# Kernel optimization log

Hardware: AMD Instinct MI355X
Metric: run time of the kernel (lower is better)

The kernel has to match this reference:

```python
import jax, jax.numpy as jnp
import numpy as np

B, T, C, H = 2, 2048, 1024, 16
D = C // H  # head_dim = 64

def setup_inputs() -> dict:
    key = jax.random.key(0)
    k1, k2, k3 = jax.random.split(key, 3)
    x = jax.random.normal(k1, (B, T, C), dtype=jnp.float32)
    W_attn = jax.random.normal(k2, (C, 3 * C), dtype=jnp.float32) * (1.0 / np.sqrt(C))
    W_proj = jax.random.normal(k3, (C, C), dtype=jnp.float32) * (1.0 / np.sqrt(C))
    return {"x": x, "W_attn": W_attn, "W_proj": W_proj}

def reference(x, W_attn, W_proj):
    b, t, c = x.shape
    qkv = x @ W_attn                       # [B,T,3C]
    q, k, v = jnp.split(qkv, 3, axis=-1)
    # [B,T,C] -> [B,H,T,D]
    q = q.reshape(b, t, H, D).transpose(0, 2, 1, 3)
    k = k.reshape(b, t, H, D).transpose(0, 2, 1, 3)
    v = v.reshape(b, t, H, D).transpose(0, 2, 1, 3)
    scale = 1.0 / np.sqrt(D).astype(np.float32)
    att = jnp.einsum('bhqd,bhkd->bhqk', q, k) * scale   # [B,H,T,T]
    causal = jnp.tril(jnp.ones((t, t), dtype=bool))
    att = jnp.where(causal[None, None], att, -jnp.inf)
    att = jax.nn.softmax(att, axis=-1)
    y = jnp.einsum('bhqk,bhkd->bhqd', att, v)           # [B,H,T,D]
    y = y.transpose(0, 2, 1, 3).reshape(b, t, c)        # [B,T,C]
    return y @ W_proj
```

## Files before the change

### kernel.cpp

```cpp
#include <hip/hip_runtime.h>
#include <hip/hip_bf16.h>
#include <cstdint>
#include <cstddef>
#include <cmath>

typedef __attribute__((ext_vector_type(8))) short short8v;
typedef __attribute__((ext_vector_type(4))) float f32x4;
typedef __attribute__((ext_vector_type(4))) unsigned short ushort4v;

__device__ __forceinline__ unsigned short f2bf(float f) {
  union { float f; uint32_t u; } v; v.f = f;
  uint32_t u = v.u;
  return (unsigned short)((u + 0x7fffu + ((u >> 16) & 1u)) >> 16);
}

__device__ __forceinline__ float bf2f(unsigned short u) {
  union { uint32_t u; float f; } v; v.u = ((uint32_t)u) << 16; return v.f;
}

__device__ __forceinline__ uint32_t pack2bf(float a, float b) {
  __hip_bfloat162 h = __float22bfloat162_rn(make_float2(a, b));
  union { __hip_bfloat162 h; uint32_t u; } c; c.h = h; return c.u;
}

__device__ __forceinline__ void load_lds_16B(const void* g, void* l) {
  __builtin_amdgcn_global_load_lds((const __attribute__((address_space(1))) void*)g,
                                   (__attribute__((address_space(3))) void*)l, 16, 0, 0);
}

__global__ __launch_bounds__(256) void cvt_bf16_kernel(const float* __restrict__ src,
                                                       unsigned short* __restrict__ dst,
                                                       int n8) {
  int i = blockIdx.x * 256 + threadIdx.x;
  if (i >= n8) return;
  const float4* s4 = (const float4*)src + (size_t)i * 2;
  float4 f0 = s4[0], f1 = s4[1];
  short8v o;
  o[0] = (short)f2bf(f0.x); o[1] = (short)f2bf(f0.y);
  o[2] = (short)f2bf(f0.z); o[3] = (short)f2bf(f0.w);
  o[4] = (short)f2bf(f1.x); o[5] = (short)f2bf(f1.y);
  o[6] = (short)f2bf(f1.z); o[7] = (short)f2bf(f1.w);
  *(short8v*)(dst + (size_t)i * 8) = o;
}

__global__ __launch_bounds__(256) void transpose_bf16_kernel(const float* __restrict__ W,
                                                             unsigned short* __restrict__ WT,
                                                             int K, int N) {
  __shared__ float tile[64][65];
  int n0 = blockIdx.x * 64, k0 = blockIdx.y * 64;
  int tid = threadIdx.x;
#pragma unroll
  for (int i = 0; i < 4; ++i) {
    int idx = i * 256 + tid;
    int r = idx >> 4, c4 = (idx & 15) * 4;
    float4 v = *(const float4*)(W + (size_t)(k0 + r) * N + n0 + c4);
    tile[r][c4] = v.x; tile[r][c4 + 1] = v.y; tile[r][c4 + 2] = v.z; tile[r][c4 + 3] = v.w;
  }
  __syncthreads();
#pragma unroll
  for (int i = 0; i < 4; ++i) {
    int idx = i * 256 + tid;
    int nr = idx >> 4, k4 = (idx & 15) * 4;
    ushort4 o;
    o.x = f2bf(tile[k4 + 0][nr]);
    o.y = f2bf(tile[k4 + 1][nr]);
    o.z = f2bf(tile[k4 + 2][nr]);
    o.w = f2bf(tile[k4 + 3][nr]);
    *(ushort4*)(WT + (size_t)(n0 + nr) * K + k0 + k4) = o;
  }
}

__global__ __launch_bounds__(256) void transpose_v_kernel(const unsigned short* __restrict__ qkv,
                                                          unsigned short* __restrict__ VT) {
  int bid = blockIdx.x;
  int b = bid >> 9, h = (bid >> 5) & 15, tc = bid & 31;
  __shared__ unsigned short tile[64][68];
  int tid = threadIdx.x;
  const unsigned short* src = qkv + (size_t)(b * 2048 + tc * 64) * 3072 + 2048 + h * 64;
#pragma unroll
  for (int p = 0; p < 4; ++p) {
    int idx = p * 256 + tid;
    int r = idx >> 4, c4 = (idx & 15) * 4;
    *(ushort4*)&tile[r][c4] = *(const ushort4*)(src + (size_t)r * 3072 + c4);
  }
  __syncthreads();
  unsigned short* dst = VT + (size_t)(b * 16 + h) * 64 * 2048 + tc * 64;
#pragma unroll
  for (int p = 0; p < 4; ++p) {
    int idx = p * 256 + tid;
    int d = idx >> 4, k = idx & 15;
    int t4 = k * 4;
    int c4 = ((k >> 3) << 5) | ((k & 3) << 3) | (k & 4);
    ushort4 o;
    o.x = tile[t4][d]; o.y = tile[t4 + 1][d]; o.z = tile[t4 + 2][d]; o.w = tile[t4 + 3][d];
    *(ushort4*)(dst + (size_t)d * 2048 + c4) = o;
  }
}

template <int BF16OUT>
__global__ __launch_bounds__(256) void gemm_bt_kernel(const unsigned short* __restrict__ A,
                                                      const unsigned short* __restrict__ BT,
                                                      void* __restrict__ Cout,
                                                      int M, int N, int K) {
  __shared__ __align__(16) char lds[32768];
  char* As = lds;
  char* Bs = lds + 16384;

  int nbn = N >> 7;
  int nwg = gridDim.x;
  int wg = blockIdx.x;
  int per = nwg >> 3;
  int swz = (wg & 7) * per + (wg >> 3);
  int tm = swz / nbn, tn = swz % nbn;

  int tid = threadIdx.x;
  int wid = tid >> 6, lane = tid & 63;
  int l15 = lane & 15, lhi = lane >> 4;
  int wm = wid >> 1, wn = wid & 1;

  const unsigned short* Abase = A + (size_t)(tm * 128) * K;
  const unsigned short* Bbase = BT + (size_t)(tn * 128) * K;

  size_t ofs[4];
#pragma unroll
  for (int i = 0; i < 4; ++i) {
    int row = i * 32 + (tid >> 3);
    int ss = (tid & 7) ^ (row & 7);
    ofs[i] = (size_t)row * K + ss * 8;
  }

  f32x4 acc[4][4] = {};

  for (int kt = 0; kt < K; kt += 64) {
    __syncthreads();
#pragma unroll
    for (int i = 0; i < 4; ++i)
      load_lds_16B(Abase + ofs[i] + kt, As + i * 4096 + tid * 16);
#pragma unroll
    for (int i = 0; i < 4; ++i)
      load_lds_16B(Bbase + ofs[i] + kt, Bs + i * 4096 + tid * 16);
    __syncthreads();

#pragma unroll
    for (int ks = 0; ks < 2; ++ks) {
      short8v af[4], bfr[4];
#pragma unroll
      for (int mi = 0; mi < 4; ++mi) {
        int row = wm * 64 + mi * 16 + l15;
        int ss = (ks * 4 + lhi) ^ (row & 7);
        af[mi] = *(const short8v*)(As + row * 128 + ss * 16);
      }
#pragma unroll
      for (int ni = 0; ni < 4; ++ni) {
        int row = wn * 64 + ni * 16 + l15;
        int ss = (ks * 4 + lhi) ^ (row & 7);
        bfr[ni] = *(const short8v*)(Bs + row * 128 + ss * 16);
      }
#pragma unroll
      for (int mi = 0; mi < 4; ++mi)
#pragma unroll
        for (int ni = 0; ni < 4; ++ni)
          acc[mi][ni] = __builtin_amdgcn_mfma_f32_16x16x32_bf16(af[mi], bfr[ni], acc[mi][ni], 0, 0, 0);
    }
  }

#pragma unroll
  for (int mi = 0; mi < 4; ++mi)
#pragma unroll
    for (int ni = 0; ni < 4; ++ni)
#pragma unroll
      for (int r = 0; r < 4; ++r) {
        int row = tm * 128 + wm * 64 + mi * 16 + lhi * 4 + r;
        int col = tn * 128 + wn * 64 + ni * 16 + l15;
        float v = acc[mi][ni][r];
        if (BF16OUT)
          ((unsigned short*)Cout)[(size_t)row * N + col] = f2bf(v);
        else
          ((float*)Cout)[(size_t)row * N + col] = v;
      }
}

__global__ __launch_bounds__(256) void gemm_bt64_kernel(const unsigned short* __restrict__ A,
                                                        const unsigned short* __restrict__ BT,
                                                        float* __restrict__ Cout,
                                                        int M, int N, int K) {
  __shared__ __align__(16) char lds[24576];
  char* As = lds;
  char* Bs = lds + 8192;

  int nbn = N >> 7;
  int nwg = gridDim.x;
  int wg = blockIdx.x;
  int per = nwg >> 3;
  int swz = (wg & 7) * per + (wg >> 3);
  int tm = swz / nbn, tn = swz % nbn;

  int tid = threadIdx.x;
  int wid = tid >> 6, lane = tid & 63;
  int l15 = lane & 15, lhi = lane >> 4;

  const unsigned short* Abase = A + (size_t)(tm * 64) * K;
  const unsigned short* Bbase = BT + (size_t)(tn * 128) * K;

  size_t ofsA[2], ofsB[4];
#pragma unroll
  for (int i = 0; i < 2; ++i) {
    int row = i * 32 + (tid >> 3);
    int ss = (tid & 7) ^ (row & 7);
    ofsA[i] = (size_t)row * K + ss * 8;
  }
#pragma unroll
  for (int i = 0; i < 4; ++i) {
    int row = i * 32 + (tid >> 3);
    int ss = (tid & 7) ^ (row & 7);
    ofsB[i] = (size_t)row * K + ss * 8;
  }

  f32x4 acc[4][2] = {};

  for (int kt = 0; kt < K; kt += 64) {
    __syncthreads();
#pragma unroll
    for (int i = 0; i < 2; ++i)
      load_lds_16B(Abase + ofsA[i] + kt, As + i * 4096 + tid * 16);
#pragma unroll
    for (int i = 0; i < 4; ++i)
      load_lds_16B(Bbase + ofsB[i] + kt, Bs + i * 4096 + tid * 16);
    __syncthreads();

#pragma unroll
    for (int ks = 0; ks < 2; ++ks) {
      short8v af[4], bfr[2];
#pragma unroll
      for (int mi = 0; mi < 4; ++mi) {
        int row = mi * 16 + l15;
        int ss = (ks * 4 + lhi) ^ (row & 7);
        af[mi] = *(const short8v*)(As + row * 128 + ss * 16);
      }
#pragma unroll
      for (int ni = 0; ni < 2; ++ni) {
        int row = wid * 32 + ni * 16 + l15;
        int ss = (ks * 4 + lhi) ^ (row & 7);
        bfr[ni] = *(const short8v*)(Bs + row * 128 + ss * 16);
      }
#pragma unroll
      for (int mi = 0; mi < 4; ++mi)
#pragma unroll
        for (int ni = 0; ni < 2; ++ni)
          acc[mi][ni] = __builtin_amdgcn_mfma_f32_16x16x32_bf16(af[mi], bfr[ni], acc[mi][ni], 0, 0, 0);
    }
  }

#pragma unroll
  for (int mi = 0; mi < 4; ++mi)
#pragma unroll
    for (int ni = 0; ni < 2; ++ni)
#pragma unroll
      for (int r = 0; r < 4; ++r) {
        int row = tm * 64 + mi * 16 + lhi * 4 + r;
        int col = tn * 128 + wid * 32 + ni * 16 + l15;
        Cout[(size_t)row * N + col] = acc[mi][ni][r];
      }
}


__device__ __forceinline__ short8v scale_q(short8v q) {
  short8v r;
#pragma unroll
  for (int j = 0; j < 8; ++j)
    r[j] = (short)f2bf(bf2f((unsigned short)q[j]) * 0.18033688f);
  return r;
}

__device__ __forceinline__ void mask_diag(f32x4 s[4], int q_abs, int k0, int lhi) {
#pragma unroll
  for (int ni = 0; ni < 4; ++ni)
#pragma unroll
    for (int r = 0; r < 4; ++r) {
      int kv = k0 + ni * 16 + lhi * 4 + r;
      if (kv > q_abs) s[ni][r] = -1e30f;
    }
}

__device__ __forceinline__ void exp_p(f32x4 s[4]) {
#pragma unroll
  for (int ni = 0; ni < 4; ++ni)
#pragma unroll
    for (int r = 0; r < 4; ++r)
      s[ni][r] = exp2f(s[ni][r]);
}

__device__ __forceinline__ void repack_pa(const f32x4 s[4], short8v pa[2]) {
#pragma unroll
  for (int ks = 0; ks < 2; ++ks) {
    union { uint32_t u[4]; short8v v; } pk;
    pk.u[0] = pack2bf(s[2 * ks][0], s[2 * ks][1]);
    pk.u[1] = pack2bf(s[2 * ks][2], s[2 * ks][3]);
    pk.u[2] = pack2bf(s[2 * ks + 1][0], s[2 * ks + 1][1]);
    pk.u[3] = pack2bf(s[2 * ks + 1][2], s[2 * ks + 1][3]);
    pa[ks] = pk.v;
  }
}

__global__ __launch_bounds__(256, 2) void attn_kernel(const unsigned short* __restrict__ qkv,
                                                      const unsigned short* __restrict__ VT,
                                                      unsigned short* __restrict__ yb) {
  const int T = 2048, LD = 3072;
  int bid = blockIdx.x;
  int xcd = bid & 7, ii = bid >> 3;
  int bh = xcd * 4 + (ii & 3);
  int j = ii >> 2;
  int b = bh >> 4, h = bh & 15;
  int qtA = j, qtB = 31 - j;

  int tid = threadIdx.x;
  int wid = tid >> 6, lane = tid & 63;
  int l15 = lane & 15, lhi = lane >> 4;

  __shared__ __align__(16) char Ks[4][8192];
  __shared__ __align__(16) char Vt[4][8192];

  union { uint32_t u[4]; short8v v; } ob;
  ob.u[0] = ob.u[1] = ob.u[2] = ob.u[3] = 0x3F803F80u;
  const short8v onesv = ob.v;

  int qrowA = qtA * 64 + wid * 16 + l15;
  int qrowB = qtB * 64 + wid * 16 + l15;
  const unsigned short* qpA = qkv + (size_t)(b * T + qrowA) * LD + h * 64;
  const unsigned short* qpB = qkv + (size_t)(b * T + qrowB) * LD + h * 64;
  short8v qfA[2], qfB[2];
  qfA[0] = scale_q(*(const short8v*)(qpA + lhi * 8));
  qfA[1] = scale_q(*(const short8v*)(qpA + 32 + lhi * 8));
  qfB[0] = scale_q(*(const short8v*)(qpB + lhi * 8));
  qfB[1] = scale_q(*(const short8v*)(qpB + 32 + lhi * 8));

  const unsigned short* kbase = qkv + (size_t)b * T * LD + 1024 + h * 64;
  const unsigned short* vtbase = VT + (size_t)(b * 16 + h) * 64 * 2048;

  f32x4 oA[4] = {}, oB[4] = {};
  f32x4 lfA = {}, lfB = {};
  int q_absA = qtA * 64 + wid * 16 + l15;
  int q_absB = qtB * 64 + wid * 16 + l15;

  int ntA64 = qtA + 1, ntB64 = qtB + 1;
  int nSuper = (ntB64 + 1) >> 1;

  auto stageK = [&](int s) {
#pragma unroll
    for (int i2 = 0; i2 < 2; ++i2) {
      int row = i2 * 32 + (tid >> 3);
      int ss = (tid & 7) ^ (row & 7);
      load_lds_16B(kbase + (size_t)(s * 64 + row) * LD + ss * 8, Ks[s & 3] + i2 * 4096 + tid * 16);
    }
  };
  auto stageV = [&](int s) {
#pragma unroll
    for (int i2 = 0; i2 < 2; ++i2) {
      int row = i2 * 32 + (tid >> 3);
      int ss = (tid & 7) ^ (row & 7);
      load_lds_16B(vtbase + (size_t)row * 2048 + s * 64 + ss * 8, Vt[s & 3] + i2 * 4096 + tid * 16);
    }
  };

  stageK(0); stageV(0);
  stageK(1); stageV(1);
  __syncthreads();

  for (int its = 0; its < nSuper; ++its) {
    int sub0 = 2 * its, sub1 = sub0 + 1;
    int k0 = sub0 * 64;
    bool actB1 = sub1 < ntB64;
    bool actA0 = sub0 < ntA64;
    bool actA1 = sub1 < ntA64;
    int p0 = sub0 + 2, p1 = sub0 + 3;
    bool pf0 = p0 < ntB64, pf1 = p1 < ntB64;

    if (pf0) { stageK(p0); stageV(p0); }
    if (pf1) { stageK(p1); stageV(p1); }

    const char* K0 = Ks[sub0 & 3];
    const char* K1 = Ks[sub1 & 3];

    f32x4 sB0[4] = {}, sB1[4] = {}, sA0[4] = {}, sA1[4] = {};
    __builtin_amdgcn_s_setprio(1);
#pragma unroll
    for (int ks = 0; ks < 2; ++ks)
#pragma unroll
      for (int ni = 0; ni < 4; ++ni) {
        int row = ni * 16 + l15;
        int sl = (ks * 4 + lhi) ^ (row & 7);
        short8v kf = *(const short8v*)(K0 + row * 128 + sl * 16);
        sB0[ni] = __builtin_amdgcn_mfma_f32_16x16x32_bf16(kf, qfB[ks], sB0[ni], 0, 0, 0);
        if (actA0) sA0[ni] = __builtin_amdgcn_mfma_f32_16x16x32_bf16(kf, qfA[ks], sA0[ni], 0, 0, 0);
      }
    if (actB1) {
#pragma unroll
      for (int ks = 0; ks < 2; ++ks)
#pragma unroll
        for (int ni = 0; ni < 4; ++ni) {
          int row = ni * 16 + l15;
          int sl = (ks * 4 + lhi) ^ (row & 7);
          short8v kf = *(const short8v*)(K1 + row * 128 + sl * 16);
          sB1[ni] = __builtin_amdgcn_mfma_f32_16x16x32_bf16(kf, qfB[ks], sB1[ni], 0, 0, 0);
          if (actA1) sA1[ni] = __builtin_amdgcn_mfma_f32_16x16x32_bf16(kf, qfA[ks], sA1[ni], 0, 0, 0);
        }
    }
    __builtin_amdgcn_s_setprio(0);

    if (sub0 == qtB) mask_diag(sB0, q_absB, k0, lhi);
    if (sub1 == qtB) mask_diag(sB1, q_absB, k0 + 64, lhi);
    exp_p(sB0);
    if (actB1) exp_p(sB1);
    if (actA0) {
      if (sub0 == qtA) mask_diag(sA0, q_absA, k0, lhi);
      if (sub1 == qtA) mask_diag(sA1, q_absA, k0 + 64, lhi);
      exp_p(sA0);
      if (actA1) exp_p(sA1);
    }

    short8v paB0[2], paB1[2], paA0[2], paA1[2];
    repack_pa(sB0, paB0);
    if (actB1) repack_pa(sB1, paB1);
    if (actA0) repack_pa(sA0, paA0);
    if (actA1) repack_pa(sA1, paA1);

    const char* V0 = Vt[sub0 & 3];
    const char* V1 = Vt[sub1 & 3];
    __builtin_amdgcn_s_setprio(1);
#pragma unroll
    for (int ks = 0; ks < 2; ++ks)
#pragma unroll
      for (int nd = 0; nd < 4; ++nd) {
        int d = nd * 16 + l15;
        int slv = (ks * 4 + lhi) ^ (d & 7);
        short8v bv = *(const short8v*)(V0 + d * 128 + slv * 16);
        oB[nd] = __builtin_amdgcn_mfma_f32_16x16x32_bf16(paB0[ks], bv, oB[nd], 0, 0, 0);
        if (actA0) oA[nd] = __builtin_amdgcn_mfma_f32_16x16x32_bf16(paA0[ks], bv, oA[nd], 0, 0, 0);
      }
#pragma unroll
    for (int ks = 0; ks < 2; ++ks) {
      lfB = __builtin_amdgcn_mfma_f32_16x16x32_bf16(paB0[ks], onesv, lfB, 0, 0, 0);
      if (actA0) lfA = __builtin_amdgcn_mfma_f32_16x16x32_bf16(paA0[ks], onesv, lfA, 0, 0, 0);
    }
    if (actB1) {
#pragma unroll
      for (int ks = 0; ks < 2; ++ks)
#pragma unroll
        for (int nd = 0; nd < 4; ++nd) {
          int d = nd * 16 + l15;
          int slv = (ks * 4 + lhi) ^ (d & 7);
          short8v bv = *(const short8v*)(V1 + d * 128 + slv * 16);
          oB[nd] = __builtin_amdgcn_mfma_f32_16x16x32_bf16(paB1[ks], bv, oB[nd], 0, 0, 0);
          if (actA1) oA[nd] = __builtin_amdgcn_mfma_f32_16x16x32_bf16(paA1[ks], bv, oA[nd], 0, 0, 0);
        }
#pragma unroll
      for (int ks = 0; ks < 2; ++ks) {
        lfB = __builtin_amdgcn_mfma_f32_16x16x32_bf16(paB1[ks], onesv, lfB, 0, 0, 0);
        if (actA1) lfA = __builtin_amdgcn_mfma_f32_16x16x32_bf16(paA1[ks], onesv, lfA, 0, 0, 0);
      }
    }
    __builtin_amdgcn_s_setprio(0);

    __syncthreads();
  }

#pragma unroll
  for (int r = 0; r < 4; ++r) {
    float invB = 1.0f / lfB[r];
    float invA = 1.0f / lfA[r];
    int qB = qtB * 64 + wid * 16 + lhi * 4 + r;
    int qA = qtA * 64 + wid * 16 + lhi * 4 + r;
#pragma unroll
    for (int nd = 0; nd < 4; ++nd) {
      yb[(size_t)(b * T + qB) * 1024 + h * 64 + nd * 16 + l15] = f2bf(oB[nd][r] * invB);
      yb[(size_t)(b * T + qA) * 1024 + h * 64 + nd * 16 + l15] = f2bf(oA[nd][r] * invA);
    }
  }
}

extern "C" void kernel_launch(void* const* d_in, const int* in_sizes, int n_in,
                              void* d_out, int out_size, void* d_ws, size_t ws_size,
                              hipStream_t stream) {
  const float* x = (const float*)d_in[0];
  const float* Wa = (const float*)d_in[1];
  const float* Wp = (const float*)d_in[2];
  float* out = (float*)d_out;

  char* ws = (char*)d_ws;
  unsigned short* xb  = (unsigned short*)(ws);
  unsigned short* VT  = (unsigned short*)(ws);
  unsigned short* WaT = (unsigned short*)(ws + (size_t)(8u  << 20));
  unsigned short* WpT = (unsigned short*)(ws + (size_t)(14u << 20));
  unsigned short* qkv = (unsigned short*)(ws + (size_t)(16u << 20));
  unsigned short* yb  = (unsigned short*)(ws + (size_t)(40u << 20));

  cvt_bf16_kernel<<<2048, 256, 0, stream>>>(x, xb, 524288);
  transpose_bf16_kernel<<<dim3(48, 16), 256, 0, stream>>>(Wa, WaT, 1024, 3072);
  transpose_bf16_kernel<<<dim3(16, 16), 256, 0, stream>>>(Wp, WpT, 1024, 1024);
  gemm_bt_kernel<1><<<dim3(768), 256, 0, stream>>>(xb, WaT, qkv, 4096, 3072, 1024);
  transpose_v_kernel<<<dim3(1024), 256, 0, stream>>>(qkv, VT);
  attn_kernel<<<dim3(512), 256, 0, stream>>>(qkv, VT, yb);
  gemm_bt64_kernel<<<dim3(512), 256, 0, stream>>>(yb, WpT, out, 4096, 1024, 1024);
}
```

Baseline: 115.9 us.

## Load K and V fragments directly from global memory, dropping LDS staging

The attention kernel no longer stages K and V tiles through shared memory with a 4-deep async prefetch ring and per-iteration barriers. Each wave now loads its K and V MFMA operands straight from global memory into registers, one 64-key tile per iteration. The min-blocks launch bound is also relaxed. This removes LDS traffic and __syncthreads, at the cost of every wave in the block re-reading the same K/V data from global/L2 with strided, unshared accesses and no software prefetch, so latency may be exposed.

```diff
diff --git a/kernel.cpp b/kernel.cpp
--- a/kernel.cpp
+++ b/kernel.cpp
@@ -302,9 +302,9 @@
   }
 }
 
-__global__ __launch_bounds__(256, 2) void attn_kernel(const unsigned short* __restrict__ qkv,
-                                                      const unsigned short* __restrict__ VT,
-                                                      unsigned short* __restrict__ yb) {
+__global__ __launch_bounds__(256) void attn_kernel(const unsigned short* __restrict__ qkv,
+                                                   const unsigned short* __restrict__ VT,
+                                                   unsigned short* __restrict__ yb) {
   const int T = 2048, LD = 3072;
   int bid = blockIdx.x;
   int xcd = bid & 7, ii = bid >> 3;
@@ -316,9 +316,6 @@
   int tid = threadIdx.x;
   int wid = tid >> 6, lane = tid & 63;
   int l15 = lane & 15, lhi = lane >> 4;
-
-  __shared__ __align__(16) char Ks[4][8192];
-  __shared__ __align__(16) char Vt[4][8192];
 
   union { uint32_t u[4]; short8v v; } ob;
   ob.u[0] = ob.u[1] = ob.u[2] = ob.u[3] = 0x3F803F80u;
@@ -334,8 +331,8 @@
   qfB[0] = scale_q(*(const short8v*)(qpB + lhi * 8));
   qfB[1] = scale_q(*(const short8v*)(qpB + 32 + lhi * 8));
 
-  const unsigned short* kbase = qkv + (size_t)b * T * LD + 1024 + h * 64;
-  const unsigned short* vtbase = VT + (size_t)(b * 16 + h) * 64 * 2048;
+  const unsigned short* kb = qkv + (size_t)b * T * LD + 1024 + h * 64 + lhi * 8;
+  const unsigned short* vb = VT + (size_t)(b * 16 + h) * 64 * 2048 + lhi * 8;
 
   f32x4 oA[4] = {}, oB[4] = {};
   f32x4 lfA = {}, lfB = {};
@@ -343,125 +340,59 @@
   int q_absB = qtB * 64 + wid * 16 + l15;
 
   int ntA64 = qtA + 1, ntB64 = qtB + 1;
-  int nSuper = (ntB64 + 1) >> 1;
-
-  auto stageK = [&](int s) {
-#pragma unroll
-    for (int i2 = 0; i2 < 2; ++i2) {
-      int row = i2 * 32 + (tid >> 3);
-      int ss = (tid & 7) ^ (row & 7);
-      load_lds_16B(kbase + (size_t)(s * 64 + row) * LD + ss * 8, Ks[s & 3] + i2 * 4096 + tid * 16);
-    }
-  };
-  auto stageV = [&](int s) {
-#pragma unroll
-    for (int i2 = 0; i2 < 2; ++i2) {
-      int row = i2 * 32 + (tid >> 3);
-      int ss = (tid & 7) ^ (row & 7);
-      load_lds_16B(vtbase + (size_t)row * 2048 + s * 64 + ss * 8, Vt[s & 3] + i2 * 4096 + tid * 16);
-    }
-  };
-
-  stageK(0); stageV(0);
-  stageK(1); stageV(1);
-  __syncthreads();
-
-  for (int its = 0; its < nSuper; ++its) {
-    int sub0 = 2 * its, sub1 = sub0 + 1;
-    int k0 = sub0 * 64;
-    bool actB1 = sub1 < ntB64;
-    bool actA0 = sub0 < ntA64;
-    bool actA1 = sub1 < ntA64;
-    int p0 = sub0 + 2, p1 = sub0 + 3;
-    bool pf0 = p0 < ntB64, pf1 = p1 < ntB64;
-
-    if (pf0) { stageK(p0); stageV(p0); }
-    if (pf1) { stageK(p1); stageV(p1); }
-
-    const char* K0 = Ks[sub0 & 3];
-    const char* K1 = Ks[sub1 & 3];
-
-    f32x4 sB0[4] = {}, sB1[4] = {}, sA0[4] = {}, sA1[4] = {};
+
+  for (int s = 0; s < ntB64; ++s) {
+    bool actA = s < ntA64;
+    int k0 = s * 64;
+
+    short8v kf[2][4];
+#pragma unroll
+    for (int ks = 0; ks < 2; ++ks)
+#pragma unroll
+      for (int ni = 0; ni < 4; ++ni)
+        kf[ks][ni] = *(const short8v*)(kb + (size_t)(k0 + ni * 16 + l15) * LD + ks * 32);
+
+    f32x4 sB[4] = {}, sA[4] = {};
     __builtin_amdgcn_s_setprio(1);
 #pragma unroll
     for (int ks = 0; ks < 2; ++ks)
 #pragma unroll
       for (int ni = 0; ni < 4; ++ni) {
-        int row = ni * 16 + l15;
-        int sl = (ks * 4 + lhi) ^ (row & 7);
-        short8v kf = *(const short8v*)(K0 + row * 128 + sl * 16);
-        sB0[ni] = __builtin_amdgcn_mfma_f32_16x16x32_bf16(kf, qfB[ks], sB0[ni], 0, 0, 0);
-        if (actA0) sA0[ni] = __builtin_amdgcn_mfma_f32_16x16x32_bf16(kf, qfA[ks], sA0[ni], 0, 0, 0);
-      }
-    if (actB1) {
-#pragma unroll
-      for (int ks = 0; ks < 2; ++ks)
-#pragma unroll
-        for (int ni = 0; ni < 4; ++ni) {
-          int row = ni * 16 + l15;
-          int sl = (ks * 4 + lhi) ^ (row & 7);
-          short8v kf = *(const short8v*)(K1 + row * 128 + sl * 16);
-          sB1[ni] = __builtin_amdgcn_mfma_f32_16x16x32_bf16(kf, qfB[ks], sB1[ni], 0, 0, 0);
-          if (actA1) sA1[ni] = __builtin_amdgcn_mfma_f32_16x16x32_bf16(kf, qfA[ks], sA1[ni], 0, 0, 0);
-        }
-    }
+        sB[ni] = __builtin_amdgcn_mfma_f32_16x16x32_bf16(kf[ks][ni], qfB[ks], sB[ni], 0, 0, 0);
+        if (actA) sA[ni] = __builtin_amdgcn_mfma_f32_16x16x32_bf16(kf[ks][ni], qfA[ks], sA[ni], 0, 0, 0);
+      }
     __builtin_amdgcn_s_setprio(0);
 
-    if (sub0 == qtB) mask_diag(sB0, q_absB, k0, lhi);
-    if (sub1 == qtB) mask_diag(sB1, q_absB, k0 + 64, lhi);
-    exp_p(sB0);
-    if (actB1) exp_p(sB1);
-    if (actA0) {
-      if (sub0 == qtA) mask_diag(sA0, q_absA, k0, lhi);
-      if (sub1 == qtA) mask_diag(sA1, q_absA, k0 + 64, lhi);
-      exp_p(sA0);
-      if (actA1) exp_p(sA1);
-    }
-
-    short8v paB0[2], paB1[2], paA0[2], paA1[2];
-    repack_pa(sB0, paB0);
-    if (actB1) repack_pa(sB1, paB1);
-    if (actA0) repack_pa(sA0, paA0);
-    if (actA1) repack_pa(sA1, paA1);
-
-    const char* V0 = Vt[sub0 & 3];
-    const char* V1 = Vt[sub1 & 3];
+    short8v vf[2][4];
+#pragma unroll
+    for (int ks = 0; ks < 2; ++ks)
+#pragma unroll
+      for (int nd = 0; nd < 4; ++nd)
+        vf[ks][nd] = *(const short8v*)(vb + (size_t)(nd * 16 + l15) * 2048 + k0 + ks * 32);
+
+    if (s == qtB) mask_diag(sB, q_absB, k0, lhi);
+    exp_p(sB);
+    if (actA) {
+      if (s == qtA) mask_diag(sA, q_absA, k0, lhi);
+      exp_p(sA);
+    }
+
+    short8v paB[2], paA[2];
+    repack_pa(sB, paB);
+    if (actA) repack_pa(sA, paA);
+
     __builtin_amdgcn_s_setprio(1);
 #pragma unroll
-    for (int ks = 0; ks < 2; ++ks)
+    for (int ks = 0; ks < 2; ++ks) {
 #pragma unroll
       for (int nd = 0; nd < 4; ++nd) {
-        int d = nd * 16 + l15;
-        int slv = (ks * 4 + lhi) ^ (d & 7);
-        short8v bv = *(const short8v*)(V0 + d * 128 + slv * 16);
-        oB[nd] = __builtin_amdgcn_mfma_f32_16x16x32_bf16(paB0[ks], bv, oB[nd], 0, 0, 0);
-        if (actA0) oA[nd] = __builtin_amdgcn_mfma_f32_16x16x32_bf16(paA0[ks], bv, oA[nd], 0, 0, 0);
-      }
-#pragma unroll
-    for (int ks = 0; ks < 2; ++ks) {
-      lfB = __builtin_amdgcn_mfma_f32_16x16x32_bf16(paB0[ks], onesv, lfB, 0, 0, 0);
-      if (actA0) lfA = __builtin_amdgcn_mfma_f32_16x16x32_bf16(paA0[ks], onesv, lfA, 0, 0, 0);
-    }
-    if (actB1) {
-#pragma unroll
-      for (int ks = 0; ks < 2; ++ks)
-#pragma unroll
-        for (int nd = 0; nd < 4; ++nd) {
-          int d = nd * 16 + l15;
-          int slv = (ks * 4 + lhi) ^ (d & 7);
-          short8v bv = *(const short8v*)(V1 + d * 128 + slv * 16);
-          oB[nd] = __builtin_amdgcn_mfma_f32_16x16x32_bf16(paB1[ks], bv, oB[nd], 0, 0, 0);
-          if (actA1) oA[nd] = __builtin_amdgcn_mfma_f32_16x16x32_bf16(paA1[ks], bv, oA[nd], 0, 0, 0);
-        }
-#pragma unroll
-      for (int ks = 0; ks < 2; ++ks) {
-        lfB = __builtin_amdgcn_mfma_f32_16x16x32_bf16(paB1[ks], onesv, lfB, 0, 0, 0);
-        if (actA1) lfA = __builtin_amdgcn_mfma_f32_16x16x32_bf16(paA1[ks], onesv, lfA, 0, 0, 0);
-      }
+        oB[nd] = __builtin_amdgcn_mfma_f32_16x16x32_bf16(paB[ks], vf[ks][nd], oB[nd], 0, 0, 0);
+        if (actA) oA[nd] = __builtin_amdgcn_mfma_f32_16x16x32_bf16(paA[ks], vf[ks][nd], oA[nd], 0, 0, 0);
+      }
+      lfB = __builtin_amdgcn_mfma_f32_16x16x32_bf16(paB[ks], onesv, lfB, 0, 0, 0);
+      if (actA) lfA = __builtin_amdgcn_mfma_f32_16x16x32_bf16(paA[ks], onesv, lfA, 0, 0, 0);
     }
     __builtin_amdgcn_s_setprio(0);
-
-    __syncthreads();
   }
 
 #pragma unroll
```

Result: slower. 168.1 us (+45.0%).
